# Performance work log

Measured on AMD Instinct MI355X. Metric: run time of the kernel, lower is better.

Reference implementation:

```python
import jax, jax.numpy as jnp
import numpy as np

B, S, H = 64, 4096, 1024
N_OPS = 8
OP_STOP_IDX = 0
MAX_STEPS = 10


def setup_inputs() -> dict:
    key = jax.random.key(0)
    ks = jax.random.split(key, 8)
    s2a = jax.random.normal(ks[0], (B, S, H), dtype=jnp.float32)
    noise = jax.random.normal(ks[1], (MAX_STEPS, B, H), dtype=jnp.float32)
    sc_res = 1.0 / np.sqrt(2 * H)
    sc_h = 1.0 / np.sqrt(H)
    W_res = jax.random.uniform(ks[2], (2 * H, H), minval=-sc_res, maxval=sc_res, dtype=jnp.float32)
    b_res = jax.random.uniform(ks[3], (H,), minval=-sc_res, maxval=sc_res, dtype=jnp.float32)
    W_op = jax.random.uniform(ks[4], (H, N_OPS), minval=-sc_h, maxval=sc_h, dtype=jnp.float32)
    b_op = jnp.zeros((N_OPS,), dtype=jnp.float32)
    W_x = jax.random.uniform(ks[5], (H, S), minval=-sc_h, maxval=sc_h, dtype=jnp.float32)
    b_x = jnp.zeros((S,), dtype=jnp.float32)
    return {"s2a_embeddings": s2a, "W_res": W_res, "b_res": b_res,
            "W_op": W_op, "b_op": b_op, "W_x": W_x, "b_x": b_x, "noise": noise}


def reference(s2a_embeddings, W_res, b_res, W_op, b_op, W_x, b_x, noise):
    batch_idx = jnp.arange(B)

    def step(carry, noise_t):
        h, done = carry
        h_n = h + noise_t * 0.01                      # [B,H]
        op_logits = h_n @ W_op + b_op                 # [B,n_ops]
        x_logits = h_n @ W_x + b_x                    # [B,S] (== x_logits[:,0,:])
        op_idx = jnp.argmax(op_logits, axis=-1)       # [B]
        ptr = jnp.minimum(jnp.argmax(x_logits, axis=-1), S - 1)
        borrowed = s2a_embeddings[batch_idx, ptr]     # [B,H] gather
        h_new = jnp.concatenate([h_n, borrowed], axis=-1) @ W_res + b_res
        h_out = jnp.where(done, h, h_new)             # freeze once stopped
        done_new = done | jnp.all(op_idx == OP_STOP_IDX)
        return (h_out, done_new), None

    h0 = jnp.zeros((B, H), dtype=s2a_embeddings.dtype)
    (h_final, _), _ = jax.lax.scan(step, (h0, jnp.array(False)), noise)
    return h_final
```

## Files before the change

kernel.cpp:

```cpp
#include <hip/hip_runtime.h>
#include <cstdint>
#include <cstddef>

#define NB    64
#define NS    4096
#define NH    1024
#define NOPSN 8
#define NSTEP 10

#define OFF_HN0  0u
#define OFF_HN1  65536u
#define OFF_HT0  131072u
#define OFF_HT1  196608u
#define OFF_H    262144u
#define OFF_CAND 327680u
#define OFF_OPP  393216u
#define OFF_CTRL 475136u

typedef float f2v  __attribute__((ext_vector_type(2)));
typedef float f4v  __attribute__((ext_vector_type(4)));
typedef float f8v  __attribute__((ext_vector_type(8)));

__device__ __forceinline__ float bcastf(float v, int l) {
  return __int_as_float(__builtin_amdgcn_readlane(__float_as_int(v), l));
}

__global__ void __launch_bounds__(1024)
init_kernel(const float* __restrict__ noise, const float* __restrict__ Wop,
            float* __restrict__ wsf)
{
  const int b = blockIdx.x, j = threadIdx.x;
  const int lane = j & 63, jg = j >> 6;
  int* ctrl = (int*)(wsf + OFF_CTRL);
  if (b == 0 && j < NSTEP) ctrl[2 + j] = 0;

  float hv = 0.01f * noise[(size_t)b * NH + j];
  (wsf + OFF_HN0)[(size_t)b * NH + j] = hv;
  (wsf + OFF_HT0)[((size_t)(j >> 1)) * 128 + b * 2 + (j & 1)] = hv;
  (wsf + OFF_H)[(size_t)b * NH + j] = 0.f;

  const float* wrp = Wop + (size_t)j * NOPSN;
  float opo[8];
  #pragma unroll
  for (int o = 0; o < 8; ++o) opo[o] = hv * wrp[o];
  #pragma unroll
  for (int off = 1; off <= 32; off <<= 1) {
    #pragma unroll
    for (int o = 0; o < 8; ++o) opo[o] += __shfl_xor(opo[o], off);
  }
  if (lane == 0) {
    float* od = (wsf + OFF_OPP) + (size_t)jg * 512 + (size_t)b * 8;
    #pragma unroll
    for (int o = 0; o < 8; ++o) od[o] = opo[o];
  }
}

__global__ void __launch_bounds__(1024, 8)
phaseA_kernel(const float* __restrict__ Wx, const float* __restrict__ bx,
              const float* __restrict__ bop, float* __restrict__ wsf, int st)
{
  __shared__ float smem[8192];
  int* ctrl = (int*)(wsf + OFF_CTRL);
  float* __restrict__ opp = wsf + OFF_OPP;
  const float* __restrict__ hnT_cur = wsf + ((st & 1) ? OFF_HT1 : OFF_HT0);

  const int tid = threadIdx.x, blk = blockIdx.x;
  const int lane = tid & 63;
  const int wv = __builtin_amdgcn_readfirstlane(tid >> 6);
  const int s0A = blk << 3;
  const int kbaseA = wv << 6;

  const float2* hb = (const float2*)hnT_cur + ((size_t)(kbaseA >> 1)) * 64 + lane;

  if (blk < NB && tid < 64) {
    const float* ob = opp + (size_t)st * 8192 + (size_t)blk * 8;
    const int o = lane & 7, jgb = lane >> 3;
    float v = ob[(size_t)jgb * 512 + o] + ob[(size_t)(jgb + 8) * 512 + o];
    v += __shfl_xor(v, 8);
    v += __shfl_xor(v, 16);
    v += __shfl_xor(v, 32);
    v += bop[o];
    float bv = bcastf(v, 0); int bo = 0;
    #pragma unroll
    for (int oo = 1; oo < 8; ++oo) {
      float vo = bcastf(v, oo);
      if (vo > bv) { bv = vo; bo = oo; }
    }
    if (lane == 0 && bo == 0) atomicAdd(&ctrl[2 + st], 1);
  }

  float acc[8];
  #pragma unroll
  for (int s = 0; s < 8; ++s) acc[s] = 0.f;

  #pragma unroll 1
  for (int c = 0; c < 4; ++c) {
    float2 hh[8];
    #pragma unroll
    for (int i = 0; i < 8; ++i) hh[i] = hb[(size_t)(c * 8 + i) * 64];
    #pragma unroll
    for (int i = 0; i < 8; ++i) {
      const int k = kbaseA + (c * 8 + i) * 2;
      const f8v w0 = *(const f8v*)(Wx + (size_t)k * NS + s0A);
      const f8v w1 = *(const f8v*)(Wx + (size_t)(k + 1) * NS + s0A);
      #pragma unroll
      for (int s = 0; s < 8; ++s)
        acc[s] += w0[s] * hh[i].x + w1[s] * hh[i].y;
    }
  }

  #pragma unroll
  for (int s = 0; s < 8; ++s)
    smem[wv * 512 + s * 64 + lane] = acc[s];
  __syncthreads();
  {
    const int s = tid >> 6, b = tid & 63;
    float val = 0.f;
    if (s < 8) {
      val = bx[s0A + s];
      #pragma unroll
      for (int w = 0; w < 16; ++w) val += smem[w * 512 + s * 64 + b];
    }
    __syncthreads();
    if (s < 8) smem[s * 64 + b] = val;
    __syncthreads();
    if (tid < 64) {
      const int bb = tid;
      float bv = smem[bb]; int bs = 0;
      #pragma unroll
      for (int s2 = 1; s2 < 8; ++s2) {
        float v2 = smem[s2 * 64 + bb];
        if (v2 > bv) { bv = v2; bs = s2; }
      }
      float2* cp = (float2*)(wsf + OFF_CAND);
      cp[bb * 512 + blk] = make_float2(bv, __int_as_float(s0A + bs));
    }
  }
}

__global__ void __launch_bounds__(1024, 8)
phaseC_kernel(const float* __restrict__ s2a,  const float* __restrict__ Wres,
              const float* __restrict__ bres, const float* __restrict__ Wop,
              const float* __restrict__ noise, float* __restrict__ out,
              float* __restrict__ wsf, int st)
{
  __shared__ float smem[2048];
  int* ctrl = (int*)(wsf + OFF_CTRL);
  float* __restrict__ h   = wsf + OFF_H;
  float* __restrict__ opp = wsf + OFF_OPP;
  const float* __restrict__ hn_cur = wsf + ((st & 1) ? OFF_HN1 : OFF_HN0);
  float* __restrict__       hn_nxt = wsf + ((st & 1) ? OFF_HN0 : OFF_HN1);
  float* __restrict__      hnT_nxt = wsf + ((st & 1) ? OFF_HT0 : OFF_HT1);

  const int tid = threadIdx.x, blk = blockIdx.x;
  const int lane = tid & 63;
  const int wv = __builtin_amdgcn_readfirstlane(tid >> 6);
  const int jg = blk & 15, bg = blk >> 4;
  const int j0 = jg << 6, b0 = bg << 1;

  int ptrs[2] = {0, 0};
  if (wv >= 8) {
    const float2* cp = (const float2*)(wsf + OFF_CAND);
    #pragma unroll
    for (int i = 0; i < 2; ++i) {
      const float2* row = cp + (size_t)(b0 + i) * 512;
      float2 c0 = row[lane];
      float bv = c0.x; int bi = __float_as_int(c0.y);
      #pragma unroll
      for (int q = 1; q < 8; ++q) {
        float2 c = row[q * 64 + lane];
        if (c.x > bv) { bv = c.x; bi = __float_as_int(c.y); }
      }
      #pragma unroll
      for (int off = 1; off <= 32; off <<= 1) {
        float ov = __shfl_xor(bv, off);
        int   oi = __shfl_xor(bi, off);
        if (ov > bv || (ov == bv && oi < bi)) { bv = ov; bi = oi; }
      }
      ptrs[i] = __builtin_amdgcn_readfirstlane(bi);
    }
  }
  int done = 0;
  for (int tt = 0; tt < st; ++tt) done |= (ctrl[2 + tt] == NB) ? 1 : 0;

  const int kb = wv << 7;
  const float *p0, *p1;
  if (wv < 8) {
    p0 = hn_cur + (size_t)(b0 + 0) * NH + kb;
    p1 = hn_cur + (size_t)(b0 + 1) * NH + kb;
  } else {
    p0 = s2a + ((size_t)(b0 + 0) * NS + ptrs[0]) * NH + (kb - NH);
    p1 = s2a + ((size_t)(b0 + 1) * NS + ptrs[1]) * NH + (kb - NH);
  }
  const float* wp = Wres + (size_t)kb * NH + j0 + lane;

  float a0 = 0.f, a1 = 0.f;

  #pragma unroll 1
  for (int kc = 0; kc < 128; kc += 8) {
    float w[8];
    f4v q0[2], q1[2];
    #pragma unroll
    for (int i = 0; i < 8; ++i) w[i] = wp[(size_t)(kc + i) * NH];
    #pragma unroll
    for (int i = 0; i < 2; ++i) {
      q0[i] = *(const f4v*)(p0 + kc + 4 * i);
      q1[i] = *(const f4v*)(p1 + kc + 4 * i);
    }
    #pragma unroll
    for (int i = 0; i < 8; ++i) {
      const float wv_ = w[i];
      a0 += q0[i >> 2][i & 3] * wv_;
      a1 += q1[i >> 2][i & 3] * wv_;
    }
  }

  smem[wv * 128 + 0 * 64 + lane] = a0;
  smem[wv * 128 + 1 * 64 + lane] = a1;
  __syncthreads();

  if (tid < 128) {
    const int bsel = tid >> 6, jloc = tid & 63;
    float v = bres[j0 + jloc];
    #pragma unroll
    for (int w = 0; w < 16; ++w) v += smem[w * 128 + bsel * 64 + jloc];
    const int b = b0 + bsel, j = j0 + jloc;
    float hold = h[(size_t)b * NH + j];
    float hout = done ? hold : v;
    h[(size_t)b * NH + j] = hout;
    if (st < NSTEP - 1) {
      float hnv = hout + 0.01f * noise[(size_t)(st + 1) * (NB * NH) + (size_t)b * NH + j];
      hn_nxt[(size_t)b * NH + j] = hnv;
      hnT_nxt[((size_t)(j >> 1)) * 128 + b * 2 + (j & 1)] = hnv;
      const float* wrp = Wop + (size_t)j * NOPSN;
      float opo[8];
      #pragma unroll
      for (int o = 0; o < 8; ++o) opo[o] = hnv * wrp[o];
      #pragma unroll
      for (int off = 1; off <= 32; off <<= 1) {
        #pragma unroll
        for (int o = 0; o < 8; ++o) opo[o] += __shfl_xor(opo[o], off);
      }
      if ((tid & 63) == 0) {
        float* od = opp + ((size_t)(st + 1) * 16 + jg) * 512 + (size_t)b * 8;
        #pragma unroll
        for (int o = 0; o < 8; ++o) od[o] = opo[o];
      }
    } else {
      out[(size_t)b * NH + j] = hout;
    }
  }
}

extern "C" void kernel_launch(void* const* d_in, const int* in_sizes, int n_in,
                              void* d_out, int out_size, void* d_ws, size_t ws_size,
                              hipStream_t stream) {
  const float* s2a   = (const float*)d_in[0];
  const float* Wres  = (const float*)d_in[1];
  const float* bres  = (const float*)d_in[2];
  const float* Wop   = (const float*)d_in[3];
  const float* bop   = (const float*)d_in[4];
  const float* Wx    = (const float*)d_in[5];
  const float* bx    = (const float*)d_in[6];
  const float* noise = (const float*)d_in[7];
  float* outp = (float*)d_out;
  float* wsf  = (float*)d_ws;

  hipLaunchKernelGGL(init_kernel, dim3(64), dim3(1024), 0, stream,
                     noise, Wop, wsf);
  for (int st = 0; st < NSTEP; ++st) {
    hipLaunchKernelGGL(phaseA_kernel, dim3(512), dim3(1024), 0, stream,
                       Wx, bx, bop, wsf, st);
    hipLaunchKernelGGL(phaseC_kernel, dim3(512), dim3(1024), 0, stream,
                       s2a, Wres, bres, Wop, noise, outp, wsf, st);
  }
}
```

Baseline: 1.670 ms.

## Retile phaseC residual GEMV to 4 batches by 32 columns per block

Changes the phaseC tile from 2 batch rows by 64 output columns to 4 batch rows by 32 columns. Each loaded W_res value is now reused across four batch rows instead of two, which halves W_res traffic per FLOP. In exchange the activation/gather loads double per column and the loads are 32-lane wide. The op-logit partial buffer goes from 16 to 32 column groups, so the workspace layout, the init kernel and the phaseA reduction are adjusted to match. The shared-memory reduction also grows to 32 partials.

After: 1.806 ms. 8.1% more time.

```diff
diff --git a/kernel.cpp b/kernel.cpp
--- a/kernel.cpp
+++ b/kernel.cpp
@@ -15,7 +15,7 @@
 #define OFF_H    262144u
 #define OFF_CAND 327680u
 #define OFF_OPP  393216u
-#define OFF_CTRL 475136u
+#define OFF_CTRL 557056u
 
 typedef float f2v  __attribute__((ext_vector_type(2)));
 typedef float f4v  __attribute__((ext_vector_type(4)));
@@ -30,7 +30,7 @@
             float* __restrict__ wsf)
 {
   const int b = blockIdx.x, j = threadIdx.x;
-  const int lane = j & 63, jg = j >> 6;
+  const int jg32 = j >> 5;
   int* ctrl = (int*)(wsf + OFF_CTRL);
   if (b == 0 && j < NSTEP) ctrl[2 + j] = 0;
 
@@ -44,12 +44,12 @@
   #pragma unroll
   for (int o = 0; o < 8; ++o) opo[o] = hv * wrp[o];
   #pragma unroll
-  for (int off = 1; off <= 32; off <<= 1) {
+  for (int off = 1; off <= 16; off <<= 1) {
     #pragma unroll
     for (int o = 0; o < 8; ++o) opo[o] += __shfl_xor(opo[o], off);
   }
-  if (lane == 0) {
-    float* od = (wsf + OFF_OPP) + (size_t)jg * 512 + (size_t)b * 8;
+  if ((j & 31) == 0) {
+    float* od = (wsf + OFF_OPP) + (size_t)jg32 * 512 + (size_t)b * 8;
     #pragma unroll
     for (int o = 0; o < 8; ++o) od[o] = opo[o];
   }
@@ -73,9 +73,12 @@
   const float2* hb = (const float2*)hnT_cur + ((size_t)(kbaseA >> 1)) * 64 + lane;
 
   if (blk < NB && tid < 64) {
-    const float* ob = opp + (size_t)st * 8192 + (size_t)blk * 8;
+    const float* ob = opp + (size_t)st * 16384 + (size_t)blk * 8;
     const int o = lane & 7, jgb = lane >> 3;
-    float v = ob[(size_t)jgb * 512 + o] + ob[(size_t)(jgb + 8) * 512 + o];
+    float v = 0.f;
+    #pragma unroll
+    for (int m = 0; m < 4; ++m)
+      v += ob[(size_t)(jgb + 8 * m) * 512 + o];
     v += __shfl_xor(v, 8);
     v += __shfl_xor(v, 16);
     v += __shfl_xor(v, 32);
@@ -144,7 +147,7 @@
               const float* __restrict__ noise, float* __restrict__ out,
               float* __restrict__ wsf, int st)
 {
-  __shared__ float smem[2048];
+  __shared__ float smem[4096];
   int* ctrl = (int*)(wsf + OFF_CTRL);
   float* __restrict__ h   = wsf + OFF_H;
   float* __restrict__ opp = wsf + OFF_OPP;
@@ -155,14 +158,14 @@
   const int tid = threadIdx.x, blk = blockIdx.x;
   const int lane = tid & 63;
   const int wv = __builtin_amdgcn_readfirstlane(tid >> 6);
-  const int jg = blk & 15, bg = blk >> 4;
-  const int j0 = jg << 6, b0 = bg << 1;
-
-  int ptrs[2] = {0, 0};
+  const int jg = blk & 31, bg = blk >> 5;
+  const int j0 = jg << 5, b0 = bg << 2;
+
+  int ptrs[4] = {0, 0, 0, 0};
   if (wv >= 8) {
     const float2* cp = (const float2*)(wsf + OFF_CAND);
     #pragma unroll
-    for (int i = 0; i < 2; ++i) {
+    for (int i = 0; i < 4; ++i) {
       const float2* row = cp + (size_t)(b0 + i) * 512;
       float2 c0 = row[lane];
       float bv = c0.x; int bi = __float_as_int(c0.y);
@@ -183,48 +186,59 @@
   int done = 0;
   for (int tt = 0; tt < st; ++tt) done |= (ctrl[2 + tt] == NB) ? 1 : 0;
 
-  const int kb = wv << 7;
-  const float *p0, *p1;
+  const int jloc = lane & 31, kh = lane >> 5;
+  const int kb = (wv << 7) + (kh << 6);
+  const float *p0, *p1, *p2, *p3;
   if (wv < 8) {
     p0 = hn_cur + (size_t)(b0 + 0) * NH + kb;
     p1 = hn_cur + (size_t)(b0 + 1) * NH + kb;
+    p2 = hn_cur + (size_t)(b0 + 2) * NH + kb;
+    p3 = hn_cur + (size_t)(b0 + 3) * NH + kb;
   } else {
     p0 = s2a + ((size_t)(b0 + 0) * NS + ptrs[0]) * NH + (kb - NH);
     p1 = s2a + ((size_t)(b0 + 1) * NS + ptrs[1]) * NH + (kb - NH);
-  }
-  const float* wp = Wres + (size_t)kb * NH + j0 + lane;
-
-  float a0 = 0.f, a1 = 0.f;
+    p2 = s2a + ((size_t)(b0 + 2) * NS + ptrs[2]) * NH + (kb - NH);
+    p3 = s2a + ((size_t)(b0 + 3) * NS + ptrs[3]) * NH + (kb - NH);
+  }
+  const float* wp = Wres + (size_t)kb * NH + j0 + jloc;
+
+  float a0 = 0.f, a1 = 0.f, a2 = 0.f, a3 = 0.f;
 
   #pragma unroll 1
-  for (int kc = 0; kc < 128; kc += 8) {
-    float w[8];
-    f4v q0[2], q1[2];
-    #pragma unroll
-    for (int i = 0; i < 8; ++i) w[i] = wp[(size_t)(kc + i) * NH];
-    #pragma unroll
-    for (int i = 0; i < 2; ++i) {
-      q0[i] = *(const f4v*)(p0 + kc + 4 * i);
-      q1[i] = *(const f4v*)(p1 + kc + 4 * i);
-    }
-    #pragma unroll
-    for (int i = 0; i < 8; ++i) {
+  for (int kc = 0; kc < 64; kc += 4) {
+    float w[4];
+    f4v q0, q1, q2, q3;
+    #pragma unroll
+    for (int i = 0; i < 4; ++i) w[i] = wp[(size_t)(kc + i) * NH];
+    q0 = *(const f4v*)(p0 + kc);
+    q1 = *(const f4v*)(p1 + kc);
+    q2 = *(const f4v*)(p2 + kc);
+    q3 = *(const f4v*)(p3 + kc);
+    #pragma unroll
+    for (int i = 0; i < 4; ++i) {
       const float wv_ = w[i];
-      a0 += q0[i >> 2][i & 3] * wv_;
-      a1 += q1[i >> 2][i & 3] * wv_;
-    }
-  }
-
-  smem[wv * 128 + 0 * 64 + lane] = a0;
-  smem[wv * 128 + 1 * 64 + lane] = a1;
+      a0 += q0[i] * wv_;
+      a1 += q1[i] * wv_;
+      a2 += q2[i] * wv_;
+      a3 += q3[i] * wv_;
+    }
+  }
+
+  {
+    const int p = (wv << 1) | kh;
+    smem[p * 128 + 0 * 32 + jloc] = a0;
+    smem[p * 128 + 1 * 32 + jloc] = a1;
+    smem[p * 128 + 2 * 32 + jloc] = a2;
+    smem[p * 128 + 3 * 32 + jloc] = a3;
+  }
   __syncthreads();
 
   if (tid < 128) {
-    const int bsel = tid >> 6, jloc = tid & 63;
-    float v = bres[j0 + jloc];
-    #pragma unroll
-    for (int w = 0; w < 16; ++w) v += smem[w * 128 + bsel * 64 + jloc];
-    const int b = b0 + bsel, j = j0 + jloc;
+    const int bsel = tid >> 5, jl = tid & 31;
+    float v = bres[j0 + jl];
+    #pragma unroll
+    for (int p = 0; p < 32; ++p) v += smem[p * 128 + bsel * 32 + jl];
+    const int b = b0 + bsel, j = j0 + jl;
     float hold = h[(size_t)b * NH + j];
     float hout = done ? hold : v;
     h[(size_t)b * NH + j] = hout;
@@ -237,12 +251,12 @@
       #pragma unroll
       for (int o = 0; o < 8; ++o) opo[o] = hnv * wrp[o];
       #pragma unroll
-      for (int off = 1; off <= 32; off <<= 1) {
+      for (int off = 1; off <= 16; off <<= 1) {
         #pragma unroll
         for (int o = 0; o < 8; ++o) opo[o] += __shfl_xor(opo[o], off);
       }
-      if ((tid & 63) == 0) {
-        float* od = opp + ((size_t)(st + 1) * 16 + jg) * 512 + (size_t)b * 8;
+      if (jl == 0) {
+        float* od = opp + ((size_t)(st + 1) * 32 + jg) * 512 + (size_t)b * 8;
         #pragma unroll
         for (int o = 0; o < 8; ++o) od[o] = opo[o];
       }
```
